# Kernel optimization log

Hardware: AMD Instinct MI355X
Metric: run time of the kernel (lower is better)

Reference implementation:

```python
import jax, jax.numpy as jnp
import numpy as np

B = 256   # batch (bs)
N = 6890  # SMPL vertices
J = 24    # joints (root + 23)
NB = 10   # betas
P = 100   # points per foot plane
PARENTS = np.array([-1,0,0,0,1,2,3,4,5,6,7,8,9,9,9,12,13,14,16,17,18,19,20,21], dtype=np.int64)


def setup_inputs() -> dict:
    key = jax.random.key(0)
    ks = jax.random.split(key, 20)
    v_template = jax.random.normal(ks[0], (N, 3), jnp.float32) * 0.3
    shapedirs = jax.random.normal(ks[1], (N, 3, NB), jnp.float32) * 0.01
    Jr = jax.random.uniform(ks[2], (J, N), jnp.float32)
    J_regressor = Jr / Jr.sum(axis=1, keepdims=True)
    lw = jax.random.uniform(ks[3], (N, J), jnp.float32)
    lbs_weights = lw / lw.sum(axis=1, keepdims=True)
    betas = jnp.concatenate([jnp.ones((1, 1), jnp.float32),
                             jax.random.normal(ks[4], (1, NB), jnp.float32) * 0.5], axis=1)
    return dict(
        v_template=v_template, shapedirs=shapedirs, J_regressor=J_regressor,
        lbs_weights=lbs_weights, betas=betas,
        body_pose_wo_foot=jax.random.normal(ks[5], (B, 57), jnp.float32) * 0.2,
        r_back_foot_pose=jax.random.normal(ks[6], (B, 3), jnp.float32) * 0.2,
        r_front_foot_pose=jax.random.normal(ks[7], (B,), jnp.float32) * 0.2,
        l_back_foot_pose=jax.random.normal(ks[8], (B, 3), jnp.float32) * 0.2,
        l_front_foot_pose=jax.random.normal(ks[9], (B,), jnp.float32) * 0.2,
        transl=jax.random.normal(ks[10], (B, 3), jnp.float32) * 0.1,
        global_orient=jax.random.normal(ks[11], (B, 3), jnp.float32) * 0.2,
        init_plane_back_l=jax.random.normal(ks[12], (B, P, 3), jnp.float32) * 0.1,
        init_plane_front_l=jax.random.normal(ks[13], (B, P, 3), jnp.float32) * 0.1,
        init_plane_back_r=jax.random.normal(ks[14], (B, P, 3), jnp.float32) * 0.1,
        init_plane_front_r=jax.random.normal(ks[15], (B, P, 3), jnp.float32) * 0.1,
        parents=jnp.asarray(PARENTS),
        foot_back_l_ids=jax.random.randint(ks[16], (P,), 0, N),
        foot_back_r_ids=jax.random.randint(ks[17], (P,), 0, N),
        foot_front_l_ids=jax.random.randint(ks[18], (P,), 0, N),
        foot_front_r_ids=jax.random.randint(ks[19], (P,), 0, N),
    )


def _rodrigues(rot_vecs):
    # rot_vecs: [M,3] axis-angle -> [M,3,3] rotation matrices (matches SMPL batch_rodrigues)
    angle = jnp.linalg.norm(rot_vecs + 1e-8, axis=1, keepdims=True)  # [M,1]
    rot_dir = rot_vecs / angle
    cos = jnp.cos(angle)[..., None]  # [M,1,1]
    sin = jnp.sin(angle)[..., None]
    rx, ry, rz = rot_dir[:, 0], rot_dir[:, 1], rot_dir[:, 2]
    zeros = jnp.zeros_like(rx)
    K = jnp.stack([zeros, -rz, ry, rz, zeros, -rx, -ry, rx, zeros], axis=1).reshape(-1, 3, 3)
    I = jnp.eye(3, dtype=rot_vecs.dtype)
    return I + sin * K + (1.0 - cos) * jnp.matmul(K, K)


def _forward(v_template, shapedirs, J_regressor, lbs_weights, betas,
             body_pose_wo_foot, r_back_foot_pose, r_front_foot_pose,
             l_back_foot_pose, l_front_foot_pose, transl, global_orient,
             init_plane_back_l, init_plane_front_l, init_plane_back_r, init_plane_front_r,
             ids):
    Bn = body_pose_wo_foot.shape[0]
    dt = v_template.dtype
    # --- update_shape ---
    blend = jnp.einsum('bl,mkl->bmk', betas[:, 1:], shapedirs)            # [1,N,3]
    v_shaped = (v_template[None] + blend) * betas[:, 0][:, None, None]    # [1,N,3]
    J_shaped = jnp.einsum('bik,ji->bjk', v_shaped, J_regressor)           # [1,J,3]
    # --- assemble full pose (foot-joint splicing) ---
    z2 = jnp.zeros((Bn, 2), dt)
    body_pose = jnp.concatenate([
        body_pose_wo_foot[:, :18],              # joints 1..6
        l_back_foot_pose,                       # joint 7
        r_back_foot_pose,                       # joint 8
        body_pose_wo_foot[:, 18:21],            # joint 9
        l_front_foot_pose[:, None], z2,         # joint 10 (x only)
        r_front_foot_pose[:, None], z2,         # joint 11 (x only)
        body_pose_wo_foot[:, 21:]], axis=1)     # joints 12..23
    full_pose = jnp.concatenate([global_orient, body_pose], axis=1)      # [B,72]
    rot = _rodrigues(full_pose.reshape(-1, 3)).reshape(Bn, J, 3, 3)
    # --- batch_rigid_transform ---
    joints = jnp.broadcast_to(J_shaped, (Bn, J, 3))
    rel = jnp.concatenate([joints[:, :1], joints[:, 1:] - joints[:, PARENTS[1:]]], axis=1)
    top = jnp.concatenate([rot, rel[..., None]], axis=-1)                 # [B,J,3,4]
    bottom = jnp.broadcast_to(jnp.array([0., 0., 0., 1.], dt), (Bn, J, 1, 4))
    T_loc = jnp.concatenate([top, bottom], axis=2)                        # [B,J,4,4]
    chain = [T_loc[:, 0]]
    for i in range(1, J):  # fixed 24-joint kinematic chain
        chain.append(chain[int(PARENTS[i])] @ T_loc[:, i])
    transforms = jnp.stack(chain, axis=1)                                 # [B,J,4,4]
    J_transformed = transforms[..., :3, 3]
    init_bone = jnp.einsum('bjmn,bjn->bjm', transforms[..., :3, :3], joints)
    A = transforms.at[..., :3, 3].add(-init_bone)                         # relative transforms
    # --- LBS skinning ---
    T = jnp.einsum('vj,bjmn->bvmn', lbs_weights, A)                       # [B,N,4,4]
    verts = jnp.einsum('bvmn,vn->bvm', T[:, :, :3, :3], v_shaped[0]) + T[:, :, :3, 3] + transl[:, None]
    # --- foot planes ---
    def _plane(idx, init):
        Tp = T[:, idx]                                                    # [B,P,4,4]
        return jnp.einsum('bpmn,bpn->bpm', Tp[:, :, :3, :3], init) + Tp[:, :, :3, 3]
    bl, fl, br, fr = ids
    v_plane = jnp.concatenate([
        _plane(bl, init_plane_back_l), _plane(fl, init_plane_front_l),
        _plane(br, init_plane_back_r), _plane(fr, init_plane_front_r)], axis=1) + transl[:, None]
    return verts, J_transformed, v_plane


def reference(v_template, shapedirs, J_regressor, lbs_weights, betas,
              body_pose_wo_foot, r_back_foot_pose, r_front_foot_pose,
              l_back_foot_pose, l_front_foot_pose, transl, global_orient,
              init_plane_back_l, init_plane_front_l, init_plane_back_r, init_plane_front_r,
              parents, foot_back_l_ids, foot_back_r_ids, foot_front_l_ids, foot_front_r_ids):
    ids = (foot_back_l_ids, foot_front_l_ids, foot_back_r_ids, foot_front_r_ids)
    return _forward(v_template, shapedirs, J_regressor, lbs_weights, betas,
                    body_pose_wo_foot, r_back_foot_pose, r_front_foot_pose,
                    l_back_foot_pose, l_front_foot_pose, transl, global_orient,
                    init_plane_back_l, init_plane_front_l, init_plane_back_r, init_plane_front_r,
                    ids)
```

## Files before the change

kernel.cpp:

```cpp
#include <hip/hip_runtime.h>
#include <stdint.h>

#define NV 6890
#define NJ 24
#define NB_ 256
#define NP 100
#define MP 6912

typedef unsigned short u16;
typedef unsigned int u32;
typedef __attribute__((ext_vector_type(8))) short bf16x8;
typedef __attribute__((ext_vector_type(4))) float f32x4;

__device__ __forceinline__ u16 f2bf(float f) {
    u32 u = __float_as_uint(f);
    u += 0x7FFFu + ((u >> 16) & 1u);
    return (u16)(u >> 16);
}

__constant__ int c_par[24] = {-1,0,0,0,1,2,3,4,5,6,7,8,9,9,9,12,13,14,16,17,18,19,20,21};

#define O_VS 0
#define O_JS 20672
#define O_A  20800
#define O_WT 189056
#define O_AT 852608

#define OUT_JT   5291520
#define OUT_PLN  5309952

__global__ __launch_bounds__(256) void k_shape(const float* __restrict__ vt,
                                               const float* __restrict__ sd,
                                               const float* __restrict__ jreg,
                                               const float* __restrict__ betas,
                                               float* __restrict__ ws) {
    int bx = blockIdx.x;
    float b0 = betas[0];
    if (bx < 81) {
        int idx = bx * 256 + threadIdx.x;
        if (idx < NV * 3) {
            float acc = vt[idx];
            const float* row = sd + (size_t)idx * 10;
#pragma unroll
            for (int l = 0; l < 10; ++l) acc += betas[1 + l] * row[l];
            ws[O_VS + idx] = acc * b0;
        }
        return;
    }
    int j = bx - 81;
    int tid = threadIdx.x;
    float be[10];
#pragma unroll
    for (int l = 0; l < 10; ++l) be[l] = betas[1 + l];
    float s0 = 0.f, s1 = 0.f, s2 = 0.f;
    for (int i = tid; i < NV; i += 256) {
        float w = jreg[(size_t)j * NV + i];
        const float* sr = sd + (size_t)i * 30;
        const float* vr = vt + (size_t)i * 3;
        float c0 = vr[0], c1 = vr[1], c2 = vr[2];
#pragma unroll
        for (int l = 0; l < 10; ++l) {
            c0 += be[l] * sr[l];
            c1 += be[l] * sr[10 + l];
            c2 += be[l] * sr[20 + l];
        }
        s0 += w * (c0 * b0);
        s1 += w * (c1 * b0);
        s2 += w * (c2 * b0);
    }
    __shared__ float r0[256], r1[256], r2[256];
    r0[tid] = s0; r1[tid] = s1; r2[tid] = s2;
    __syncthreads();
    for (int off = 128; off > 0; off >>= 1) {
        if (tid < off) { r0[tid] += r0[tid + off]; r1[tid] += r1[tid + off]; r2[tid] += r2[tid + off]; }
        __syncthreads();
    }
    if (tid == 0) {
        ws[O_JS + j * 3 + 0] = r0[0];
        ws[O_JS + j * 3 + 1] = r1[0];
        ws[O_JS + j * 3 + 2] = r2[0];
    }
}

__global__ __launch_bounds__(256) void k_prep(const float* __restrict__ lw,
                                              const float* __restrict__ bpwf,
                                              const float* __restrict__ rback,
                                              const float* __restrict__ rfront,
                                              const float* __restrict__ lback,
                                              const float* __restrict__ lfront,
                                              const float* __restrict__ gor,
                                              float* __restrict__ ws,
                                              u16* __restrict__ wsu,
                                              float* __restrict__ out) {
    int bx = blockIdx.x;
    if (bx < 2592) {
        int idx = bx * 256 + threadIdx.x;
        int v = idx / 96, k = idx - 96 * v;
        u16 o = 0;
        if (v < NV) {
            int j = k >> 2, n = k & 3;
            float w = lw[(size_t)v * 24 + j];
            float h = (n < 3) ? ws[O_VS + v * 3 + n] : 1.0f;
            o = f2bf(w * h);
        }
        wsu[O_WT + idx] = o;
        return;
    }
    int b = bx - 2592;
    int j = threadIdx.x;
    const float* js = ws + O_JS;
    __shared__ float sT[24][12];
    __shared__ float sJ[24][3];
    if (j < 24) {
        float px, py, pz;
        if (j == 0)      { px = gor[b*3];   py = gor[b*3+1];   pz = gor[b*3+2]; }
        else if (j <= 6) { int o = b*57 + 3*(j-1); px = bpwf[o]; py = bpwf[o+1]; pz = bpwf[o+2]; }
        else if (j == 7) { px = lback[b*3]; py = lback[b*3+1]; pz = lback[b*3+2]; }
        else if (j == 8) { px = rback[b*3]; py = rback[b*3+1]; pz = rback[b*3+2]; }
        else if (j == 9) { int o = b*57 + 18;     px = bpwf[o]; py = bpwf[o+1]; pz = bpwf[o+2]; }
        else if (j == 10){ px = lfront[b];  py = 0.f; pz = 0.f; }
        else if (j == 11){ px = rfront[b];  py = 0.f; pz = 0.f; }
        else             { int o = b*57 + 21 + 3*(j-12); px = bpwf[o]; py = bpwf[o+1]; pz = bpwf[o+2]; }
        float ax = px + 1e-8f, ay = py + 1e-8f, az = pz + 1e-8f;
        float ang = sqrtf(ax*ax + ay*ay + az*az);
        float inv = 1.0f / ang;
        float dx = px * inv, dy = py * inv, dz = pz * inv;
        float c = cosf(ang), s = sinf(ang), t = 1.0f - c;
        sJ[j][0] = js[j*3]; sJ[j][1] = js[j*3+1]; sJ[j][2] = js[j*3+2];
        int p = c_par[j];
        float rx = sJ[j][0], ry = sJ[j][1], rz = sJ[j][2];
        if (p >= 0) { rx -= js[p*3]; ry -= js[p*3+1]; rz -= js[p*3+2]; }
        sT[j][0] = 1.f - t*(dy*dy + dz*dz);
        sT[j][1] = -s*dz + t*dx*dy;
        sT[j][2] =  s*dy + t*dx*dz;
        sT[j][3] = rx;
        sT[j][4] =  s*dz + t*dx*dy;
        sT[j][5] = 1.f - t*(dx*dx + dz*dz);
        sT[j][6] = -s*dx + t*dy*dz;
        sT[j][7] = ry;
        sT[j][8] = -s*dy + t*dx*dz;
        sT[j][9] =  s*dx + t*dy*dz;
        sT[j][10]= 1.f - t*(dx*dx + dy*dy);
        sT[j][11]= rz;
    }
    __syncthreads();
    if (j < 24) {
        int path[12]; int d = 0; int cur = j;
        while (cur >= 0) { path[d++] = cur; cur = c_par[cur]; }
        float g[12];
        int r = path[d - 1];
#pragma unroll
        for (int m = 0; m < 12; ++m) g[m] = sT[r][m];
        for (int i = d - 2; i >= 0; --i) {
            int n = path[i];
            float h[12];
#pragma unroll
            for (int row = 0; row < 3; ++row) {
                float a0 = g[row*4+0], a1 = g[row*4+1], a2 = g[row*4+2], a3 = g[row*4+3];
                h[row*4+0] = a0*sT[n][0] + a1*sT[n][4] + a2*sT[n][8];
                h[row*4+1] = a0*sT[n][1] + a1*sT[n][5] + a2*sT[n][9];
                h[row*4+2] = a0*sT[n][2] + a1*sT[n][6] + a2*sT[n][10];
                h[row*4+3] = a0*sT[n][3] + a1*sT[n][7] + a2*sT[n][11] + a3;
            }
#pragma unroll
            for (int m = 0; m < 12; ++m) g[m] = h[m];
        }
        size_t jo = (size_t)OUT_JT + ((size_t)b * 24 + j) * 3;
        out[jo+0] = g[3]; out[jo+1] = g[7]; out[jo+2] = g[11];
        float jx = sJ[j][0], jy = sJ[j][1], jz = sJ[j][2];
        float Av[12];
        Av[0]=g[0]; Av[1]=g[1]; Av[2]=g[2];   Av[3] = g[3]  - (g[0]*jx + g[1]*jy + g[2]*jz);
        Av[4]=g[4]; Av[5]=g[5]; Av[6]=g[6];   Av[7] = g[7]  - (g[4]*jx + g[5]*jy + g[6]*jz);
        Av[8]=g[8]; Av[9]=g[9]; Av[10]=g[10]; Av[11]= g[11] - (g[8]*jx + g[9]*jy + g[10]*jz);
        float* Ab = ws + O_A + ((size_t)b * 24 + j) * 12;
#pragma unroll
        for (int m = 0; m < 12; ++m) Ab[m] = Av[m];
        u16* at = wsu + O_AT;
#pragma unroll
        for (int m = 0; m < 3; ++m)
#pragma unroll
            for (int n = 0; n < 4; ++n)
                at[(size_t)(b*3 + m) * 96 + j*4 + n] = f2bf(Av[m*4 + n]);
    }
}

__global__ __launch_bounds__(256) void k_main(const u16* __restrict__ wsu,
                                              const float* __restrict__ ws,
                                              const float* __restrict__ lw,
                                              const float* __restrict__ transl,
                                              const int* __restrict__ ids_bl,
                                              const int* __restrict__ ids_fl,
                                              const int* __restrict__ ids_br,
                                              const int* __restrict__ ids_fr,
                                              const float* __restrict__ ip_bl,
                                              const float* __restrict__ ip_fl,
                                              const float* __restrict__ ip_br,
                                              const float* __restrict__ ip_fr,
                                              float* __restrict__ out) {
    if (blockIdx.y < 12) {
        __shared__ float ltile[64][66];
        const u16* wt = wsu + O_WT;
        const u16* at = wsu + O_AT;
        int lane = threadIdx.x & 63;
        int wave = threadIdx.x >> 6;
        int row_in = lane & 15, quad = lane >> 4;
        int v0 = blockIdx.x * 64 + wave * 16;
        int c0 = blockIdx.y * 64;

        f32x4 acc0 = {0.f,0.f,0.f,0.f}, acc1 = acc0, acc2 = acc0, acc3 = acc0;
#pragma unroll
        for (int kc = 0; kc < 96; kc += 32) {
            bf16x8 a  = *(const bf16x8*)(wt + (size_t)(v0 + row_in) * 96 + kc + quad * 8);
            bf16x8 b0 = *(const bf16x8*)(at + (size_t)(c0 +  0 + row_in) * 96 + kc + quad * 8);
            bf16x8 b1 = *(const bf16x8*)(at + (size_t)(c0 + 16 + row_in) * 96 + kc + quad * 8);
            bf16x8 b2 = *(const bf16x8*)(at + (size_t)(c0 + 32 + row_in) * 96 + kc + quad * 8);
            bf16x8 b3 = *(const bf16x8*)(at + (size_t)(c0 + 48 + row_in) * 96 + kc + quad * 8);
            acc0 = __builtin_amdgcn_mfma_f32_16x16x32_bf16(a, b0, acc0, 0, 0, 0);
            acc1 = __builtin_amdgcn_mfma_f32_16x16x32_bf16(a, b1, acc1, 0, 0, 0);
            acc2 = __builtin_amdgcn_mfma_f32_16x16x32_bf16(a, b2, acc2, 0, 0, 0);
            acc3 = __builtin_amdgcn_mfma_f32_16x16x32_bf16(a, b3, acc3, 0, 0, 0);
        }
        int vbase = wave * 16 + quad * 4;
#pragma unroll
        for (int s = 0; s < 4; ++s) {
            f32x4 acc = (s == 0) ? acc0 : (s == 1) ? acc1 : (s == 2) ? acc2 : acc3;
#pragma unroll
            for (int r = 0; r < 4; ++r)
                ltile[vbase + r][s * 16 + row_in] = acc[r];
        }
        __syncthreads();
        int vblk = blockIdx.x * 64;
        int bstart = c0 / 3;
        int bend = (c0 + 63) / 3;
        int tid = threadIdx.x;
        for (int b = bstart; b <= bend; ++b) {
            if (tid < 192) {
                int vl = tid / 3, m = tid - 3 * (tid / 3);
                int cl = b * 3 + m - c0;
                int v = vblk + vl;
                if (cl >= 0 && cl < 64 && v < NV)
                    out[((size_t)b * NV + v) * 3 + m] = ltile[vl][cl] + transl[b * 3 + m];
            }
            if (tid >= 192 && tid < 192 + 64) {
            }
        }
        return;
    }
    for (int idx = blockIdx.x * 256 + threadIdx.x; idx < NB_ * 400; idx += 108 * 256) {
        int b = idx / 400;
        int rr = idx - 400 * b;
        int plane = rr / 100;
        int p = rr - 100 * plane;
        const int* ids   = (plane == 0) ? ids_bl : (plane == 1) ? ids_fl : (plane == 2) ? ids_br : ids_fr;
        const float* ip  = (plane == 0) ? ip_bl  : (plane == 1) ? ip_fl  : (plane == 2) ? ip_br  : ip_fr;
        int vid = ids[p];
        const float* Ab = ws + O_A + (size_t)b * 288;
        const float* w = lw + (size_t)vid * 24;
        float T[12];
#pragma unroll
        for (int m = 0; m < 12; ++m) T[m] = 0.f;
#pragma unroll
        for (int j = 0; j < NJ; ++j) {
            float wj = w[j];
#pragma unroll
            for (int m = 0; m < 12; ++m) T[m] += wj * Ab[j * 12 + m];
        }
        size_t io = ((size_t)b * NP + p) * 3;
        float vx = ip[io+0], vy = ip[io+1], vz = ip[io+2];
        float ox = T[0]*vx + T[1]*vy + T[2]*vz  + T[3]  + transl[b*3+0];
        float oy = T[4]*vx + T[5]*vy + T[6]*vz  + T[7]  + transl[b*3+1];
        float oz = T[8]*vx + T[9]*vy + T[10]*vz + T[11] + transl[b*3+2];
        size_t o = (size_t)OUT_PLN + (size_t)idx * 3;
        out[o+0] = ox; out[o+1] = oy; out[o+2] = oz;
    }
}

extern "C" void kernel_launch(void* const* d_in, const int* in_sizes, int n_in,
                              void* d_out, int out_size, void* d_ws, size_t ws_size,
                              hipStream_t stream) {
    const float* vt     = (const float*)d_in[0];
    const float* sd     = (const float*)d_in[1];
    const float* jreg   = (const float*)d_in[2];
    const float* lw     = (const float*)d_in[3];
    const float* betas  = (const float*)d_in[4];
    const float* bpwf   = (const float*)d_in[5];
    const float* rback  = (const float*)d_in[6];
    const float* rfront = (const float*)d_in[7];
    const float* lback  = (const float*)d_in[8];
    const float* lfront = (const float*)d_in[9];
    const float* transl = (const float*)d_in[10];
    const float* gor    = (const float*)d_in[11];
    const float* ip_bl  = (const float*)d_in[12];
    const float* ip_fl  = (const float*)d_in[13];
    const float* ip_br  = (const float*)d_in[14];
    const float* ip_fr  = (const float*)d_in[15];
    const int* ids_bl = (const int*)d_in[17];
    const int* ids_br = (const int*)d_in[18];
    const int* ids_fl = (const int*)d_in[19];
    const int* ids_fr = (const int*)d_in[20];

    float* ws  = (float*)d_ws;
    u16*   wsu = (u16*)d_ws;
    float* out = (float*)d_out;

    k_shape<<<dim3(81 + 24), 256, 0, stream>>>(vt, sd, jreg, betas, ws);
    k_prep <<<dim3(2592 + 256), 256, 0, stream>>>(lw, bpwf, rback, rfront, lback, lfront, gor,
                                                  ws, wsu, out);
    k_main <<<dim3(108, 13), 256, 0, stream>>>(wsu, ws, lw, transl,
                                               ids_bl, ids_fl, ids_br, ids_fr,
                                               ip_bl, ip_fl, ip_br, ip_fr, out);
}
```

Baseline: 147.8 us.

## Fuse kinematic chain into GEMM blocks and cut the pipeline to two launches

Collapses three kernels into two. The shaped-vertex and joint regression are merged into one prep kernel that writes the bf16 weight matrix with vectorized stores and pre-gathers foot-plane skinning weights. The per-batch kinematic chain is now recomputed inside each GEMM, plane and joint block and kept in shared memory, instead of being written to global memory and read back. This removes a launch and the global round-trip for the transforms, at the cost of redundant rodrigues and chain work in every block.

```diff
diff --git a/kernel.cpp b/kernel.cpp
--- a/kernel.cpp
+++ b/kernel.cpp
@@ -7,6 +7,13 @@
 #define NP 100
 #define MP 6912
 
+#define OUT_JT   5291520
+#define OUT_PLN  5309952
+
+#define O_JS 0
+#define O_PW 128
+#define O_WT 32768
+
 typedef unsigned short u16;
 typedef unsigned int u32;
 typedef __attribute__((ext_vector_type(8))) short bf16x8;
@@ -20,242 +27,272 @@
 
 __constant__ int c_par[24] = {-1,0,0,0,1,2,3,4,5,6,7,8,9,9,9,12,13,14,16,17,18,19,20,21};
 
-#define O_VS 0
-#define O_JS 20672
-#define O_A  20800
-#define O_WT 189056
-#define O_AT 852608
-
-#define OUT_JT   5291520
-#define OUT_PLN  5309952
-
-__global__ __launch_bounds__(256) void k_shape(const float* __restrict__ vt,
-                                               const float* __restrict__ sd,
-                                               const float* __restrict__ jreg,
-                                               const float* __restrict__ betas,
-                                               float* __restrict__ ws) {
-    int bx = blockIdx.x;
-    float b0 = betas[0];
-    if (bx < 81) {
-        int idx = bx * 256 + threadIdx.x;
-        if (idx < NV * 3) {
-            float acc = vt[idx];
-            const float* row = sd + (size_t)idx * 10;
-#pragma unroll
-            for (int l = 0; l < 10; ++l) acc += betas[1 + l] * row[l];
-            ws[O_VS + idx] = acc * b0;
+struct Params {
+    const float *vt, *sd, *jreg, *lw, *betas, *bpwf, *rback, *rfront,
+                *lback, *lfront, *transl, *gor, *ip_bl, *ip_fl, *ip_br, *ip_fr;
+    const int *ids_bl, *ids_fl, *ids_br, *ids_fr;
+    float* ws;
+    u16* wsu;
+    float* out;
+};
+
+__device__ __forceinline__ void chain_part1(const Params& P, const float* js,
+                                            float* sTq, int b, int jj) {
+    float px, py, pz;
+    const float* bp = P.bpwf;
+    if (jj == 0)      { px = P.gor[b*3];   py = P.gor[b*3+1];   pz = P.gor[b*3+2]; }
+    else if (jj <= 6) { int o = b*57 + 3*(jj-1); px = bp[o]; py = bp[o+1]; pz = bp[o+2]; }
+    else if (jj == 7) { px = P.lback[b*3]; py = P.lback[b*3+1]; pz = P.lback[b*3+2]; }
+    else if (jj == 8) { px = P.rback[b*3]; py = P.rback[b*3+1]; pz = P.rback[b*3+2]; }
+    else if (jj == 9) { int o = b*57 + 18;     px = bp[o]; py = bp[o+1]; pz = bp[o+2]; }
+    else if (jj == 10){ px = P.lfront[b];  py = 0.f; pz = 0.f; }
+    else if (jj == 11){ px = P.rfront[b];  py = 0.f; pz = 0.f; }
+    else              { int o = b*57 + 21 + 3*(jj-12); px = bp[o]; py = bp[o+1]; pz = bp[o+2]; }
+    float ax = px + 1e-8f, ay = py + 1e-8f, az = pz + 1e-8f;
+    float ang = sqrtf(ax*ax + ay*ay + az*az);
+    float inv = 1.0f / ang;
+    float dx = px * inv, dy = py * inv, dz = pz * inv;
+    float c = cosf(ang), s = sinf(ang), t = 1.0f - c;
+    int p = c_par[jj];
+    float rx = js[jj*3+0], ry = js[jj*3+1], rz = js[jj*3+2];
+    if (p >= 0) { rx -= js[p*3]; ry -= js[p*3+1]; rz -= js[p*3+2]; }
+    sTq[jj*12+0] = 1.f - t*(dy*dy + dz*dz);
+    sTq[jj*12+1] = -s*dz + t*dx*dy;
+    sTq[jj*12+2] =  s*dy + t*dx*dz;
+    sTq[jj*12+3] = rx;
+    sTq[jj*12+4] =  s*dz + t*dx*dy;
+    sTq[jj*12+5] = 1.f - t*(dx*dx + dz*dz);
+    sTq[jj*12+6] = -s*dx + t*dy*dz;
+    sTq[jj*12+7] = ry;
+    sTq[jj*12+8] = -s*dy + t*dx*dz;
+    sTq[jj*12+9] =  s*dx + t*dy*dz;
+    sTq[jj*12+10]= 1.f - t*(dx*dx + dy*dy);
+    sTq[jj*12+11]= rz;
+}
+__device__ __forceinline__ void chain_part2(const float* sTq, float* g, int jj) {
+    int path[12]; int d = 0; int cur = jj;
+    while (cur >= 0) { path[d++] = cur; cur = c_par[cur]; }
+    int r = path[d - 1];
+#pragma unroll
+    for (int m = 0; m < 12; ++m) g[m] = sTq[r*12+m];
+    for (int i = d - 2; i >= 0; --i) {
+        int n = path[i];
+        float h[12];
+#pragma unroll
+        for (int row = 0; row < 3; ++row) {
+            float a0 = g[row*4+0], a1 = g[row*4+1], a2 = g[row*4+2], a3 = g[row*4+3];
+            h[row*4+0] = a0*sTq[n*12+0] + a1*sTq[n*12+4] + a2*sTq[n*12+8];
+            h[row*4+1] = a0*sTq[n*12+1] + a1*sTq[n*12+5] + a2*sTq[n*12+9];
+            h[row*4+2] = a0*sTq[n*12+2] + a1*sTq[n*12+6] + a2*sTq[n*12+10];
+            h[row*4+3] = a0*sTq[n*12+3] + a1*sTq[n*12+7] + a2*sTq[n*12+11] + a3;
+        }
+#pragma unroll
+        for (int m = 0; m < 12; ++m) g[m] = h[m];
+    }
+}
+
+__global__ __launch_bounds__(256) void k_pre(Params P) {
+    int bx = blockIdx.x, tid = threadIdx.x;
+    if (bx < 24) {
+        int j = bx;
+        __shared__ float sb[11];
+        __shared__ float r0[256], r1[256], r2[256];
+        if (tid < 11) sb[tid] = P.betas[tid];
+        __syncthreads();
+        float s0 = 0.f, s1 = 0.f, s2 = 0.f;
+        const float* jr = P.jreg + (size_t)j * NV;
+        for (int q = tid; q < 206700; q += 256) {
+            float x = P.sd[q];
+            int i = q / 30; int cc = q - 30 * i;
+            int n = (cc >= 20) ? 2 : ((cc >= 10) ? 1 : 0);
+            int l = cc - 10 * n;
+            float t = jr[i] * sb[1 + l] * x;
+            s0 += (n == 0) ? t : 0.f;
+            s1 += (n == 1) ? t : 0.f;
+            s2 += (n == 2) ? t : 0.f;
+        }
+        for (int q = tid; q < 20670; q += 256) {
+            float x = P.vt[q];
+            int i = q / 3; int n = q - 3 * i;
+            float t = jr[i] * x;
+            s0 += (n == 0) ? t : 0.f;
+            s1 += (n == 1) ? t : 0.f;
+            s2 += (n == 2) ? t : 0.f;
+        }
+        r0[tid] = s0; r1[tid] = s1; r2[tid] = s2;
+        __syncthreads();
+        for (int off = 128; off > 0; off >>= 1) {
+            if (tid < off) { r0[tid] += r0[tid+off]; r1[tid] += r1[tid+off]; r2[tid] += r2[tid+off]; }
+            __syncthreads();
+        }
+        if (tid == 0) {
+            float b0 = sb[0];
+            P.ws[O_JS + j*3 + 0] = b0 * r0[0];
+            P.ws[O_JS + j*3 + 1] = b0 * r1[0];
+            P.ws[O_JS + j*3 + 2] = b0 * r2[0];
         }
         return;
     }
-    int j = bx - 81;
-    int tid = threadIdx.x;
-    float be[10];
-#pragma unroll
-    for (int l = 0; l < 10; ++l) be[l] = betas[1 + l];
-    float s0 = 0.f, s1 = 0.f, s2 = 0.f;
-    for (int i = tid; i < NV; i += 256) {
-        float w = jreg[(size_t)j * NV + i];
-        const float* sr = sd + (size_t)i * 30;
-        const float* vr = vt + (size_t)i * 3;
-        float c0 = vr[0], c1 = vr[1], c2 = vr[2];
-#pragma unroll
-        for (int l = 0; l < 10; ++l) {
-            c0 += be[l] * sr[l];
-            c1 += be[l] * sr[10 + l];
-            c2 += be[l] * sr[20 + l];
-        }
-        s0 += w * (c0 * b0);
-        s1 += w * (c1 * b0);
-        s2 += w * (c2 * b0);
-    }
-    __shared__ float r0[256], r1[256], r2[256];
-    r0[tid] = s0; r1[tid] = s1; r2[tid] = s2;
-    __syncthreads();
-    for (int off = 128; off > 0; off >>= 1) {
-        if (tid < off) { r0[tid] += r0[tid + off]; r1[tid] += r1[tid + off]; r2[tid] += r2[tid + off]; }
-        __syncthreads();
-    }
-    if (tid == 0) {
-        ws[O_JS + j * 3 + 0] = r0[0];
-        ws[O_JS + j * 3 + 1] = r1[0];
-        ws[O_JS + j * 3 + 2] = r2[0];
-    }
-}
-
-__global__ __launch_bounds__(256) void k_prep(const float* __restrict__ lw,
-                                              const float* __restrict__ bpwf,
-                                              const float* __restrict__ rback,
-                                              const float* __restrict__ rfront,
-                                              const float* __restrict__ lback,
-                                              const float* __restrict__ lfront,
-                                              const float* __restrict__ gor,
-                                              float* __restrict__ ws,
-                                              u16* __restrict__ wsu,
-                                              float* __restrict__ out) {
-    int bx = blockIdx.x;
-    if (bx < 2592) {
-        int idx = bx * 256 + threadIdx.x;
-        int v = idx / 96, k = idx - 96 * v;
-        u16 o = 0;
+    if (bx < 51) {
+        int v = (bx - 24) * 256 + tid;
+        u16 buf[96];
         if (v < NV) {
-            int j = k >> 2, n = k & 3;
-            float w = lw[(size_t)v * 24 + j];
-            float h = (n < 3) ? ws[O_VS + v * 3 + n] : 1.0f;
-            o = f2bf(w * h);
-        }
-        wsu[O_WT + idx] = o;
+            float be[11];
+#pragma unroll
+            for (int l = 0; l < 11; ++l) be[l] = P.betas[l];
+            const float* sr = P.sd + (size_t)v * 30;
+            const float* vr = P.vt + (size_t)v * 3;
+            float vs[3];
+#pragma unroll
+            for (int n = 0; n < 3; ++n) {
+                float acc = vr[n];
+#pragma unroll
+                for (int l = 0; l < 10; ++l) acc += be[1 + l] * sr[n * 10 + l];
+                vs[n] = acc * be[0];
+            }
+            const float* wr = P.lw + (size_t)v * 24;
+#pragma unroll
+            for (int j = 0; j < 24; ++j) {
+                float w = wr[j];
+                buf[j*4+0] = f2bf(w * vs[0]);
+                buf[j*4+1] = f2bf(w * vs[1]);
+                buf[j*4+2] = f2bf(w * vs[2]);
+                buf[j*4+3] = f2bf(w);
+            }
+        } else {
+#pragma unroll
+            for (int m = 0; m < 96; ++m) buf[m] = 0;
+        }
+        uint4* dst = (uint4*)(P.wsu + O_WT + (size_t)v * 96);
+        const uint4* src = (const uint4*)buf;
+#pragma unroll
+        for (int m = 0; m < 12; ++m) dst[m] = src[m];
         return;
     }
-    int b = bx - 2592;
-    int j = threadIdx.x;
-    const float* js = ws + O_JS;
-    __shared__ float sT[24][12];
-    __shared__ float sJ[24][3];
-    if (j < 24) {
-        float px, py, pz;
-        if (j == 0)      { px = gor[b*3];   py = gor[b*3+1];   pz = gor[b*3+2]; }
-        else if (j <= 6) { int o = b*57 + 3*(j-1); px = bpwf[o]; py = bpwf[o+1]; pz = bpwf[o+2]; }
-        else if (j == 7) { px = lback[b*3]; py = lback[b*3+1]; pz = lback[b*3+2]; }
-        else if (j == 8) { px = rback[b*3]; py = rback[b*3+1]; pz = rback[b*3+2]; }
-        else if (j == 9) { int o = b*57 + 18;     px = bpwf[o]; py = bpwf[o+1]; pz = bpwf[o+2]; }
-        else if (j == 10){ px = lfront[b];  py = 0.f; pz = 0.f; }
-        else if (j == 11){ px = rfront[b];  py = 0.f; pz = 0.f; }
-        else             { int o = b*57 + 21 + 3*(j-12); px = bpwf[o]; py = bpwf[o+1]; pz = bpwf[o+2]; }
-        float ax = px + 1e-8f, ay = py + 1e-8f, az = pz + 1e-8f;
-        float ang = sqrtf(ax*ax + ay*ay + az*az);
-        float inv = 1.0f / ang;
-        float dx = px * inv, dy = py * inv, dz = pz * inv;
-        float c = cosf(ang), s = sinf(ang), t = 1.0f - c;
-        sJ[j][0] = js[j*3]; sJ[j][1] = js[j*3+1]; sJ[j][2] = js[j*3+2];
-        int p = c_par[j];
-        float rx = sJ[j][0], ry = sJ[j][1], rz = sJ[j][2];
-        if (p >= 0) { rx -= js[p*3]; ry -= js[p*3+1]; rz -= js[p*3+2]; }
-        sT[j][0] = 1.f - t*(dy*dy + dz*dz);
-        sT[j][1] = -s*dz + t*dx*dy;
-        sT[j][2] =  s*dy + t*dx*dz;
-        sT[j][3] = rx;
-        sT[j][4] =  s*dz + t*dx*dy;
-        sT[j][5] = 1.f - t*(dx*dx + dz*dz);
-        sT[j][6] = -s*dx + t*dy*dz;
-        sT[j][7] = ry;
-        sT[j][8] = -s*dy + t*dx*dz;
-        sT[j][9] =  s*dx + t*dy*dz;
-        sT[j][10]= 1.f - t*(dx*dx + dy*dy);
-        sT[j][11]= rz;
-    }
-    __syncthreads();
-    if (j < 24) {
-        int path[12]; int d = 0; int cur = j;
-        while (cur >= 0) { path[d++] = cur; cur = c_par[cur]; }
-        float g[12];
-        int r = path[d - 1];
-#pragma unroll
-        for (int m = 0; m < 12; ++m) g[m] = sT[r][m];
-        for (int i = d - 2; i >= 0; --i) {
-            int n = path[i];
-            float h[12];
-#pragma unroll
-            for (int row = 0; row < 3; ++row) {
-                float a0 = g[row*4+0], a1 = g[row*4+1], a2 = g[row*4+2], a3 = g[row*4+3];
-                h[row*4+0] = a0*sT[n][0] + a1*sT[n][4] + a2*sT[n][8];
-                h[row*4+1] = a0*sT[n][1] + a1*sT[n][5] + a2*sT[n][9];
-                h[row*4+2] = a0*sT[n][2] + a1*sT[n][6] + a2*sT[n][10];
-                h[row*4+3] = a0*sT[n][3] + a1*sT[n][7] + a2*sT[n][11] + a3;
+    int q = (bx - 51) * 256 + tid;
+    if (q < 9600) {
+        int rr = q / 24, j = q - 24 * rr;
+        int plane = rr / 100, p = rr - 100 * plane;
+        const int* ids = (plane == 0) ? P.ids_bl : (plane == 1) ? P.ids_fl
+                       : (plane == 2) ? P.ids_br : P.ids_fr;
+        P.ws[O_PW + q] = P.lw[(size_t)ids[p] * 24 + j];
+    }
+}
+
+#define N_GEMM 1296
+#define N_PLN  400
+#define N_JT   32
+
+__global__ __launch_bounds__(256) void k_mainv2(Params P) {
+    __shared__ __align__(16) char smem[28704];
+    int bx = blockIdx.x, tid = threadIdx.x;
+
+    if (bx < N_GEMM) {
+        u16*   at_u  = (u16*)smem;
+        float* ltile = (float*)smem;
+        float* sT    = (float*)(smem + 16896);
+        float* js    = (float*)(smem + 28416);
+        int tx = bx % 108, ty = bx / 108;
+        int c0 = ty * 64;
+        int bstart = c0 / 3;
+        int bend = (c0 + 63) / 3;
+        int nb = bend - bstart + 1;
+        if (tid < 72) js[tid] = P.ws[O_JS + tid];
+        int g = tid / 24, jj = tid - 24 * g;
+        for (int r = 0; r < 3; ++r) {
+            int q = r * 10 + g;
+            bool act = (tid < 240) && (q < nb);
+            __syncthreads();
+            if (act) chain_part1(P, js, sT + q % 10 * 0 + g * 288, bstart + q, jj);
+            __syncthreads();
+            if (act) {
+                float gg[12];
+                chain_part2(sT + g * 288, gg, jj);
+                float jx = js[jj*3+0], jy = js[jj*3+1], jz = js[jj*3+2];
+                float Av[12];
+                Av[0]=gg[0]; Av[1]=gg[1]; Av[2]=gg[2];   Av[3] = gg[3]  - (gg[0]*jx + gg[1]*jy + gg[2]*jz);
+                Av[4]=gg[4]; Av[5]=gg[5]; Av[6]=gg[6];   Av[7] = gg[7]  - (gg[4]*jx + gg[5]*jy + gg[6]*jz);
+                Av[8]=gg[8]; Av[9]=gg[9]; Av[10]=gg[10]; Av[11]= gg[11] - (gg[8]*jx + gg[9]*jy + gg[10]*jz);
+                int b = bstart + q;
+#pragma unroll
+                for (int m = 0; m < 3; ++m) {
+                    int row = b * 3 + m - c0;
+                    if (row >= 0 && row < 64) {
+#pragma unroll
+                        for (int n = 0; n < 4; ++n)
+                            at_u[row * 96 + jj * 4 + n] = f2bf(Av[m*4 + n]);
+                    }
+                }
             }
-#pragma unroll
-            for (int m = 0; m < 12; ++m) g[m] = h[m];
-        }
-        size_t jo = (size_t)OUT_JT + ((size_t)b * 24 + j) * 3;
-        out[jo+0] = g[3]; out[jo+1] = g[7]; out[jo+2] = g[11];
-        float jx = sJ[j][0], jy = sJ[j][1], jz = sJ[j][2];
-        float Av[12];
-        Av[0]=g[0]; Av[1]=g[1]; Av[2]=g[2];   Av[3] = g[3]  - (g[0]*jx + g[1]*jy + g[2]*jz);
-        Av[4]=g[4]; Av[5]=g[5]; Av[6]=g[6];   Av[7] = g[7]  - (g[4]*jx + g[5]*jy + g[6]*jz);
-        Av[8]=g[8]; Av[9]=g[9]; Av[10]=g[10]; Av[11]= g[11] - (g[8]*jx + g[9]*jy + g[10]*jz);
-        float* Ab = ws + O_A + ((size_t)b * 24 + j) * 12;
-#pragma unroll
-        for (int m = 0; m < 12; ++m) Ab[m] = Av[m];
-        u16* at = wsu + O_AT;
-#pragma unroll
-        for (int m = 0; m < 3; ++m)
-#pragma unroll
-            for (int n = 0; n < 4; ++n)
-                at[(size_t)(b*3 + m) * 96 + j*4 + n] = f2bf(Av[m*4 + n]);
-    }
-}
-
-__global__ __launch_bounds__(256) void k_main(const u16* __restrict__ wsu,
-                                              const float* __restrict__ ws,
-                                              const float* __restrict__ lw,
-                                              const float* __restrict__ transl,
-                                              const int* __restrict__ ids_bl,
-                                              const int* __restrict__ ids_fl,
-                                              const int* __restrict__ ids_br,
-                                              const int* __restrict__ ids_fr,
-                                              const float* __restrict__ ip_bl,
-                                              const float* __restrict__ ip_fl,
-                                              const float* __restrict__ ip_br,
-                                              const float* __restrict__ ip_fr,
-                                              float* __restrict__ out) {
-    if (blockIdx.y < 12) {
-        __shared__ float ltile[64][66];
-        const u16* wt = wsu + O_WT;
-        const u16* at = wsu + O_AT;
-        int lane = threadIdx.x & 63;
-        int wave = threadIdx.x >> 6;
+        }
+        __syncthreads();
+        const u16* wt = P.wsu + O_WT;
+        int lane = tid & 63, wave = tid >> 6;
         int row_in = lane & 15, quad = lane >> 4;
-        int v0 = blockIdx.x * 64 + wave * 16;
-        int c0 = blockIdx.y * 64;
-
+        int v0 = tx * 64 + wave * 16;
         f32x4 acc0 = {0.f,0.f,0.f,0.f}, acc1 = acc0, acc2 = acc0, acc3 = acc0;
 #pragma unroll
         for (int kc = 0; kc < 96; kc += 32) {
             bf16x8 a  = *(const bf16x8*)(wt + (size_t)(v0 + row_in) * 96 + kc + quad * 8);
-            bf16x8 b0 = *(const bf16x8*)(at + (size_t)(c0 +  0 + row_in) * 96 + kc + quad * 8);
-            bf16x8 b1 = *(const bf16x8*)(at + (size_t)(c0 + 16 + row_in) * 96 + kc + quad * 8);
-            bf16x8 b2 = *(const bf16x8*)(at + (size_t)(c0 + 32 + row_in) * 96 + kc + quad * 8);
-            bf16x8 b3 = *(const bf16x8*)(at + (size_t)(c0 + 48 + row_in) * 96 + kc + quad * 8);
+            bf16x8 b0 = *(const bf16x8*)(at_u + ( 0 + row_in) * 96 + kc + quad * 8);
+            bf16x8 b1 = *(const bf16x8*)(at_u + (16 + row_in) * 96 + kc + quad * 8);
+            bf16x8 b2 = *(const bf16x8*)(at_u + (32 + row_in) * 96 + kc + quad * 8);
+            bf16x8 b3 = *(const bf16x8*)(at_u + (48 + row_in) * 96 + kc + quad * 8);
             acc0 = __builtin_amdgcn_mfma_f32_16x16x32_bf16(a, b0, acc0, 0, 0, 0);
             acc1 = __builtin_amdgcn_mfma_f32_16x16x32_bf16(a, b1, acc1, 0, 0, 0);
             acc2 = __builtin_amdgcn_mfma_f32_16x16x32_bf16(a, b2, acc2, 0, 0, 0);
             acc3 = __builtin_amdgcn_mfma_f32_16x16x32_bf16(a, b3, acc3, 0, 0, 0);
         }
+        __syncthreads();
         int vbase = wave * 16 + quad * 4;
 #pragma unroll
         for (int s = 0; s < 4; ++s) {
             f32x4 acc = (s == 0) ? acc0 : (s == 1) ? acc1 : (s == 2) ? acc2 : acc3;
 #pragma unroll
             for (int r = 0; r < 4; ++r)
-                ltile[vbase + r][s * 16 + row_in] = acc[r];
-        }
-        __syncthreads();
-        int vblk = blockIdx.x * 64;
-        int bstart = c0 / 3;
-        int bend = (c0 + 63) / 3;
-        int tid = threadIdx.x;
+                ltile[(vbase + r) * 66 + s * 16 + row_in] = acc[r];
+        }
+        __syncthreads();
+        int vblk = tx * 64;
         for (int b = bstart; b <= bend; ++b) {
             if (tid < 192) {
                 int vl = tid / 3, m = tid - 3 * (tid / 3);
                 int cl = b * 3 + m - c0;
                 int v = vblk + vl;
                 if (cl >= 0 && cl < 64 && v < NV)
-                    out[((size_t)b * NV + v) * 3 + m] = ltile[vl][cl] + transl[b * 3 + m];
+                    P.out[((size_t)b * NV + v) * 3 + m] = ltile[vl * 66 + cl] + P.transl[b * 3 + m];
             }
-            if (tid >= 192 && tid < 192 + 64) {
-            }
         }
         return;
     }
-    for (int idx = blockIdx.x * 256 + threadIdx.x; idx < NB_ * 400; idx += 108 * 256) {
-        int b = idx / 400;
-        int rr = idx - 400 * b;
-        int plane = rr / 100;
-        int p = rr - 100 * plane;
-        const int* ids   = (plane == 0) ? ids_bl : (plane == 1) ? ids_fl : (plane == 2) ? ids_br : ids_fr;
-        const float* ip  = (plane == 0) ? ip_bl  : (plane == 1) ? ip_fl  : (plane == 2) ? ip_br  : ip_fr;
-        int vid = ids[p];
-        const float* Ab = ws + O_A + (size_t)b * 288;
-        const float* w = lw + (size_t)vid * 24;
+    if (bx < N_GEMM + N_PLN) {
+        float* sT2 = (float*)smem;
+        float* sAv = (float*)(smem + 2304);
+        float* js  = (float*)(smem + 4608);
+        int p0 = (bx - N_GEMM) * 256;
+        int b0 = p0 / 400;
+        int b1 = (p0 + 255) / 400;
+        if (tid < 72) js[tid] = P.ws[O_JS + tid];
+        int g = tid >> 5, jj = tid & 31;
+        bool act = (g < 2) && (jj < 24) && (g == 0 || b1 > b0);
+        __syncthreads();
+        if (act) chain_part1(P, js, sT2 + g * 288, b0 + g, jj);
+        __syncthreads();
+        if (act) {
+            float gg[12];
+            chain_part2(sT2 + g * 288, gg, jj);
+            float jx = js[jj*3+0], jy = js[jj*3+1], jz = js[jj*3+2];
+            float* A = sAv + g * 288 + jj * 12;
+            A[0]=gg[0]; A[1]=gg[1]; A[2]=gg[2];   A[3] = gg[3]  - (gg[0]*jx + gg[1]*jy + gg[2]*jz);
+            A[4]=gg[4]; A[5]=gg[5]; A[6]=gg[6];   A[7] = gg[7]  - (gg[4]*jx + gg[5]*jy + gg[6]*jz);
+            A[8]=gg[8]; A[9]=gg[9]; A[10]=gg[10]; A[11]= gg[11] - (gg[8]*jx + gg[9]*jy + gg[10]*jz);
+        }
+        __syncthreads();
+        int pt = p0 + tid;
+        int b = pt / 400;
+        int rr = pt - 400 * b;
+        const float* w  = P.ws + O_PW + rr * 24;
+        const float* Ab = sAv + (b - b0) * 288;
         float T[12];
 #pragma unroll
         for (int m = 0; m < 12; ++m) T[m] = 0.f;
@@ -265,48 +302,65 @@
 #pragma unroll
             for (int m = 0; m < 12; ++m) T[m] += wj * Ab[j * 12 + m];
         }
+        int plane = rr / 100, p = rr - 100 * plane;
+        const float* ip = (plane == 0) ? P.ip_bl : (plane == 1) ? P.ip_fl
+                        : (plane == 2) ? P.ip_br : P.ip_fr;
         size_t io = ((size_t)b * NP + p) * 3;
         float vx = ip[io+0], vy = ip[io+1], vz = ip[io+2];
-        float ox = T[0]*vx + T[1]*vy + T[2]*vz  + T[3]  + transl[b*3+0];
-        float oy = T[4]*vx + T[5]*vy + T[6]*vz  + T[7]  + transl[b*3+1];
-        float oz = T[8]*vx + T[9]*vy + T[10]*vz + T[11] + transl[b*3+2];
-        size_t o = (size_t)OUT_PLN + (size_t)idx * 3;
-        out[o+0] = ox; out[o+1] = oy; out[o+2] = oz;
+        float ox = T[0]*vx + T[1]*vy + T[2]*vz  + T[3]  + P.transl[b*3+0];
+        float oy = T[4]*vx + T[5]*vy + T[6]*vz  + T[7]  + P.transl[b*3+1];
+        float oz = T[8]*vx + T[9]*vy + T[10]*vz + T[11] + P.transl[b*3+2];
+        size_t o = (size_t)OUT_PLN + (size_t)pt * 3;
+        P.out[o+0] = ox; P.out[o+1] = oy; P.out[o+2] = oz;
+        return;
+    }
+    {
+        float* sT = (float*)smem;
+        float* js = (float*)(smem + 9216);
+        int bb0 = (bx - N_GEMM - N_PLN) * 8;
+        if (tid < 72) js[tid] = P.ws[O_JS + tid];
+        int g = tid / 24, jj = tid - 24 * g;
+        bool act = (tid < 192);
+        __syncthreads();
+        if (act) chain_part1(P, js, sT + g * 288, bb0 + g, jj);
+        __syncthreads();
+        if (act) {
+            float gg[12];
+            chain_part2(sT + g * 288, gg, jj);
+            size_t jo = (size_t)OUT_JT + ((size_t)(bb0 + g) * 24 + jj) * 3;
+            P.out[jo+0] = gg[3]; P.out[jo+1] = gg[7]; P.out[jo+2] = gg[11];
+        }
     }
 }
 
 extern "C" void kernel_launch(void* const* d_in, const int* in_sizes, int n_in,
                               void* d_out, int out_size, void* d_ws, size_t ws_size,
                               hipStream_t stream) {
-    const float* vt     = (const float*)d_in[0];
-    const float* sd     = (const float*)d_in[1];
-    const float* jreg   = (const float*)d_in[2];
-    const float* lw     = (const float*)d_in[3];
-    const float* betas  = (const float*)d_in[4];
-    const float* bpwf   = (const float*)d_in[5];
-    const float* rback  = (const float*)d_in[6];
-    const float* rfront = (const float*)d_in[7];
-    const float* lback  = (const float*)d_in[8];
-    const float* lfront = (const float*)d_in[9];
-    const float* transl = (const float*)d_in[10];
-    const float* gor    = (const float*)d_in[11];
-    const float* ip_bl  = (const float*)d_in[12];
-    const float* ip_fl  = (const float*)d_in[13];
-    const float* ip_br  = (const float*)d_in[14];
-    const float* ip_fr  = (const float*)d_in[15];
-    const int* ids_bl = (const int*)d_in[17];
-    const int* ids_br = (const int*)d_in[18];
-    const int* ids_fl = (const int*)d_in[19];
-    const int* ids_fr = (const int*)d_in[20];
-
-    float* ws  = (float*)d_ws;
-    u16*   wsu = (u16*)d_ws;
-    float* out = (float*)d_out;
-
-    k_shape<<<dim3(81 + 24), 256, 0, stream>>>(vt, sd, jreg, betas, ws);
-    k_prep <<<dim3(2592 + 256), 256, 0, stream>>>(lw, bpwf, rback, rfront, lback, lfront, gor,
-                                                  ws, wsu, out);
-    k_main <<<dim3(108, 13), 256, 0, stream>>>(wsu, ws, lw, transl,
-                                               ids_bl, ids_fl, ids_br, ids_fr,
-                                               ip_bl, ip_fl, ip_br, ip_fr, out);
-}
+    Params P;
+    P.vt     = (const float*)d_in[0];
+    P.sd     = (const float*)d_in[1];
+    P.jreg   = (const float*)d_in[2];
+    P.lw     = (const float*)d_in[3];
+    P.betas  = (const float*)d_in[4];
+    P.bpwf   = (const float*)d_in[5];
+    P.rback  = (const float*)d_in[6];
+    P.rfront = (const float*)d_in[7];
+    P.lback  = (const float*)d_in[8];
+    P.lfront = (const float*)d_in[9];
+    P.transl = (const float*)d_in[10];
+    P.gor    = (const float*)d_in[11];
+    P.ip_bl  = (const float*)d_in[12];
+    P.ip_fl  = (const float*)d_in[13];
+    P.ip_br  = (const float*)d_in[14];
+    P.ip_fr  = (const float*)d_in[15];
+    P.ids_bl = (const int*)d_in[17];
+    P.ids_br = (const int*)d_in[18];
+    P.ids_fl = (const int*)d_in[19];
+    P.ids_fr = (const int*)d_in[20];
+    P.ws  = (float*)d_ws;
+    P.wsu = (u16*)d_ws;
+    P.out = (float*)d_out;
+
+    k_pre   <<<dim3(89), 256, 0, stream>>>(P);
+    k_mainv2<<<dim3(N_GEMM + N_PLN + N_JT), 256, 0, stream>>>(P);
+}
```

Result: slower. 430.3 us (+191.2%).
